# Kernel tuning notes

Hardware: AMD Instinct MI355X
Metric: run time of the kernel (lower is better)

The kernel has to match this reference:

```python
import jax, jax.numpy as jnp
import numpy as np

N_NODES = 100000
N_EDGES = 1600000
IN_F, OUT_F = 25, 50


def setup_inputs() -> dict:
    key = jax.random.key(0)
    k1, k2, k3, k4 = jax.random.split(key, 4)
    x = jax.random.normal(k1, (N_NODES, IN_F), dtype=jnp.float32)
    W = jax.random.normal(k2, (IN_F, OUT_F), dtype=jnp.float32) * (1.0 / np.sqrt(IN_F))
    b = jax.random.normal(k3, (OUT_F,), dtype=jnp.float32) * 0.01
    edge_index = jax.random.randint(k4, (2, N_EDGES), 0, N_NODES, dtype=jnp.int64)
    return {"x": x, "W": W, "b": b, "edge_index": edge_index}


def reference(x, W, b, edge_index):
    # GCNConv(normalize=False): linear transform, then add-aggregate over edges, + bias.
    src, dst = edge_index[0], edge_index[1]
    h = x @ W                                   # [N, OUT_F] small dense GEMM
    msgs = h[src]                               # [E, OUT_F] irregular gather
    agg = jax.ops.segment_sum(msgs, dst, num_segments=N_NODES)  # scatter-add to targets
    out = agg + b
    return jax.nn.relu(out)
```

## Files before the change

### kernel.cpp

```cpp
#include <hip/hip_runtime.h>

#define N_NODES 100000
#define N_EDGES 1600000
#define IN_F 25
#define OUT_F 50

#define BNODES 98
#define NBUCK 1024
#define DL_SHIFT 7
#define SLAB 1920
#define BIN_NB 98
#define BIN_CHUNK 16384
#define XPREP_ITEMS (N_NODES * 16)
#define PREP_GRID 512

__global__ __launch_bounds__(1024) void gcn_prep_kernel(
        const float* __restrict__ x,
        const int* __restrict__ ei,
        int* __restrict__ gfill,
        unsigned* __restrict__ recs,
        unsigned* __restrict__ xb) {
    __shared__ int lcnt[NBUCK];
    __shared__ int lbase[NBUCK];
    int tid = threadIdx.x, bid = blockIdx.x;
    if (bid < BIN_NB) {
        for (int i = tid; i < NBUCK; i += 1024) lcnt[i] = 0;
        __syncthreads();
        const int4* s4 = (const int4*)ei;
        const int4* d4 = (const int4*)(ei + N_EDGES);
        int base4 = bid * (BIN_CHUNK / 4);
        int4 sv[4], dv[4];
        bool ok[4];
#pragma unroll
        for (int k = 0; k < 4; ++k) {
            int i4 = base4 + k * 1024 + tid;
            ok[k] = (i4 < N_EDGES / 4);
            if (ok[k]) { dv[k] = d4[i4]; sv[k] = s4[i4]; }
        }
#pragma unroll
        for (int k = 0; k < 4; ++k) {
            if (ok[k]) {
                const int* dd = &dv[k].x;
#pragma unroll
                for (int c = 0; c < 4; ++c)
                    atomicAdd(&lcnt[((unsigned)dd[c]) / BNODES], 1);
            }
        }
        __syncthreads();
        for (int i = tid; i < NBUCK; i += 1024) {
            int c = lcnt[i];
            lbase[i] = c ? atomicAdd(&gfill[i], c) : 0;
            lcnt[i] = 0;
        }
        __syncthreads();
#pragma unroll
        for (int k = 0; k < 4; ++k) {
            if (ok[k]) {
                const int* dd = &dv[k].x;
                const int* ss = &sv[k].x;
#pragma unroll
                for (int c = 0; c < 4; ++c) {
                    unsigned d = (unsigned)dd[c], s = (unsigned)ss[c];
                    unsigned bk = d / BNODES;
                    unsigned dl = d - bk * BNODES;
                    int p = lbase[bk] + atomicAdd(&lcnt[bk], 1);
                    if ((unsigned)p < SLAB)
                        recs[bk * SLAB + p] = (s << DL_SHIFT) | dl;
                }
            }
        }
    } else {
        for (int idx = (bid - BIN_NB) * 1024 + tid; idx < XPREP_ITEMS;
             idx += (PREP_GRID - BIN_NB) * 1024) {
            int n  = idx >> 4;
            int fp = (idx & 15) * 2;
            float v0 = (fp < IN_F) ? x[n * IN_F + fp] : 0.f;
            float v1 = (fp + 1 < IN_F) ? x[n * IN_F + fp + 1] : 0.f;
            union { float fl; unsigned u; } a, c;
            a.fl = v0; c.fl = v1;
            unsigned r0 = (a.u + 0x7FFFu + ((a.u >> 16) & 1u)) >> 16;
            unsigned r1 = (c.u + 0x7FFFu + ((c.u >> 16) & 1u)) >> 16;
            xb[idx] = (r1 << 16) | (r0 & 0xFFFFu);
        }
    }
}

__global__ __launch_bounds__(512, 8) void gcn_k3_kernel(
        const uint4* __restrict__ xb4,
        const unsigned* __restrict__ recs,
        const int* __restrict__ gfill,
        const float* __restrict__ W,
        const float* __restrict__ b,
        float* __restrict__ out) {
    __shared__ unsigned raw[SLAB];
    __shared__ int      srt[SLAB];
    __shared__ int      cnt[128], fil[128];
    __shared__ int      offs[BNODES + 1];
    __shared__ float    acc[BNODES * IN_F];
    __shared__ float    Ws[IN_F * OUT_F];
    __shared__ float    bs[OUT_F];

    int bk = blockIdx.x, tid = threadIdx.x;
    if (tid < 128) { cnt[tid] = 0; fil[tid] = 0; }
    for (int i = tid; i < IN_F * OUT_F; i += 512) Ws[i] = W[i];
    if (tid < OUT_F) bs[tid] = b[tid];
    __syncthreads();

    int cntE = min(gfill[bk], SLAB);
    const unsigned* rb = recs + bk * SLAB;

    for (int j = tid; j < cntE; j += 512) {
        unsigned rec = rb[j];
        raw[j] = rec;
        atomicAdd(&cnt[rec & ((1 << DL_SHIFT) - 1)], 1);
    }
    __syncthreads();

    if (tid < 64) {
        int v = cnt[tid];
        for (int off = 1; off < 64; off <<= 1) {
            int t = __shfl_up(v, off, 64);
            if (tid >= off) v += t;
        }
        offs[tid + 1] = v;
        int t64 = __shfl(v, 63, 64);
        int v2 = (tid < BNODES - 64) ? cnt[64 + tid] : 0;
        for (int off = 1; off < 64; off <<= 1) {
            int t = __shfl_up(v2, off, 64);
            if (tid >= off) v2 += t;
        }
        if (tid < BNODES - 64) offs[65 + tid] = t64 + v2;
        if (tid == 0) offs[0] = 0;
    }
    __syncthreads();

    for (int j = tid; j < cntE; j += 512) {
        unsigned rec = raw[j];
        int dl = rec & ((1 << DL_SHIFT) - 1);
        int p = offs[dl] + atomicAdd(&fil[dl], 1);
        srt[p] = (int)(rec >> DL_SHIFT);
    }
    __syncthreads();

    {
        int g = tid >> 2, f = tid & 3;
        if (g < BNODES) {
            int e0 = offs[g], e1 = offs[g + 1];
            float a0 = 0.f, a1 = 0.f, a2 = 0.f, a3 = 0.f;
            float a4 = 0.f, a5 = 0.f, a6 = 0.f, a7 = 0.f;
            int j = e0;
            for (; j + 4 <= e1; j += 4) {
                uint4 u[4];
#pragma unroll
                for (int q = 0; q < 4; ++q) u[q] = xb4[srt[j + q] * 4 + f];
#pragma unroll
                for (int q = 0; q < 4; ++q) {
                    union { unsigned uu; float fl; } t0, t1, t2, t3, t4, t5, t6, t7;
                    t0.uu = u[q].x << 16; t1.uu = u[q].x & 0xFFFF0000u;
                    t2.uu = u[q].y << 16; t3.uu = u[q].y & 0xFFFF0000u;
                    t4.uu = u[q].z << 16; t5.uu = u[q].z & 0xFFFF0000u;
                    t6.uu = u[q].w << 16; t7.uu = u[q].w & 0xFFFF0000u;
                    a0 += t0.fl; a1 += t1.fl; a2 += t2.fl; a3 += t3.fl;
                    a4 += t4.fl; a5 += t5.fl; a6 += t6.fl; a7 += t7.fl;
                }
            }
            for (; j < e1; ++j) {
                uint4 u = xb4[srt[j] * 4 + f];
                union { unsigned uu; float fl; } t0, t1, t2, t3, t4, t5, t6, t7;
                t0.uu = u.x << 16; t1.uu = u.x & 0xFFFF0000u;
                t2.uu = u.y << 16; t3.uu = u.y & 0xFFFF0000u;
                t4.uu = u.z << 16; t5.uu = u.z & 0xFFFF0000u;
                t6.uu = u.w << 16; t7.uu = u.w & 0xFFFF0000u;
                a0 += t0.fl; a1 += t1.fl; a2 += t2.fl; a3 += t3.fl;
                a4 += t4.fl; a5 += t5.fl; a6 += t6.fl; a7 += t7.fl;
            }
            int ff = 8 * f;
            float av[8] = {a0, a1, a2, a3, a4, a5, a6, a7};
#pragma unroll
            for (int k = 0; k < 8; ++k)
                if (ff + k < IN_F) acc[g * IN_F + ff + k] = av[k];
        }
    }
    __syncthreads();

    int node0 = bk * BNODES;
    for (int i = tid; i < BNODES * OUT_F; i += 512) {
        int nl = i / OUT_F;
        int o  = i - nl * OUT_F;
        int node = node0 + nl;
        if (node < N_NODES) {
            float a = bs[o];
#pragma unroll
            for (int k = 0; k < IN_F; ++k)
                a += acc[nl * IN_F + k] * Ws[k * OUT_F + o];
            out[node * OUT_F + o] = fmaxf(a, 0.f);
        }
    }
}

extern "C" void kernel_launch(void* const* d_in, const int* in_sizes, int n_in,
                              void* d_out, int out_size, void* d_ws, size_t ws_size,
                              hipStream_t stream) {
    const float* x  = (const float*)d_in[0];
    const float* W  = (const float*)d_in[1];
    const float* b  = (const float*)d_in[2];
    const int*   ei = (const int*)d_in[3];
    float* out = (float*)d_out;

    char* ws = (char*)d_ws;
    unsigned* xb    = (unsigned*)(ws);
    unsigned* recs  = (unsigned*)(ws + 6400000);
    int*      gfill = (int*)(ws + 14264576);

    hipMemsetAsync(gfill, 0, NBUCK * sizeof(int), stream);
    gcn_prep_kernel<<<PREP_GRID, 1024, 0, stream>>>(x, ei, gfill, recs, xb);
    gcn_k3_kernel<<<NBUCK, 512, 0, stream>>>((const uint4*)xb, recs, gfill, W, b, out);
}
```

Before: 128.5 us.

## Register-tile final GEMM with padded float4 weights and rebalance edge binning blocks

The final dense transform now has each thread compute a 2-node by 4-output tile, reading weights as float4 from a shared copy padded to 52 columns and storing results as float2. This cuts shared-memory loads and the per-element divide compared with the old one-output-per-thread loop. Edge binning is also spread across 128 blocks of 3125 int4 slots instead of 98 blocks of 4096, which balances load and frees the tail. The risk is more register pressure in the epilogue and fewer blocks left for the x-to-bf16 conversion.

Measured after the change: 358.6 us. 179% more time.

```diff
diff --git a/kernel.cpp b/kernel.cpp
--- a/kernel.cpp
+++ b/kernel.cpp
@@ -9,10 +9,12 @@
 #define NBUCK 1024
 #define DL_SHIFT 7
 #define SLAB 1920
-#define BIN_NB 98
-#define BIN_CHUNK 16384
+#define BIN_NB 128
+#define I4_TOTAL (N_EDGES / 4)
+#define I4_PER_BLK 3125
 #define XPREP_ITEMS (N_NODES * 16)
 #define PREP_GRID 512
+#define WPAD 52
 
 __global__ __launch_bounds__(1024) void gcn_prep_kernel(
         const float* __restrict__ x,
@@ -28,14 +30,14 @@
         __syncthreads();
         const int4* s4 = (const int4*)ei;
         const int4* d4 = (const int4*)(ei + N_EDGES);
-        int base4 = bid * (BIN_CHUNK / 4);
+        int base4 = bid * I4_PER_BLK;
         int4 sv[4], dv[4];
         bool ok[4];
 #pragma unroll
         for (int k = 0; k < 4; ++k) {
-            int i4 = base4 + k * 1024 + tid;
-            ok[k] = (i4 < N_EDGES / 4);
-            if (ok[k]) { dv[k] = d4[i4]; sv[k] = s4[i4]; }
+            int slot = k * 1024 + tid;
+            ok[k] = (slot < I4_PER_BLK);
+            if (ok[k]) { dv[k] = d4[base4 + slot]; sv[k] = s4[base4 + slot]; }
         }
 #pragma unroll
         for (int k = 0; k < 4; ++k) {
@@ -97,13 +99,16 @@
     __shared__ int      cnt[128], fil[128];
     __shared__ int      offs[BNODES + 1];
     __shared__ float    acc[BNODES * IN_F];
-    __shared__ float    Ws[IN_F * OUT_F];
-    __shared__ float    bs[OUT_F];
+    __shared__ __align__(16) float Ws[IN_F * WPAD];
+    __shared__ float    bs[WPAD];
 
     int bk = blockIdx.x, tid = threadIdx.x;
     if (tid < 128) { cnt[tid] = 0; fil[tid] = 0; }
-    for (int i = tid; i < IN_F * OUT_F; i += 512) Ws[i] = W[i];
-    if (tid < OUT_F) bs[tid] = b[tid];
+    for (int i = tid; i < IN_F * WPAD; i += 512) {
+        int r = i / WPAD, c = i - r * WPAD;
+        Ws[i] = (c < OUT_F) ? W[r * OUT_F + c] : 0.f;
+    }
+    if (tid < WPAD) bs[tid] = (tid < OUT_F) ? b[tid] : 0.f;
     __syncthreads();
 
     int cntE = min(gfill[bk], SLAB);
@@ -184,16 +189,40 @@
     __syncthreads();
 
     int node0 = bk * BNODES;
-    for (int i = tid; i < BNODES * OUT_F; i += 512) {
-        int nl = i / OUT_F;
-        int o  = i - nl * OUT_F;
-        int node = node0 + nl;
-        if (node < N_NODES) {
-            float a = bs[o];
-#pragma unroll
-            for (int k = 0; k < IN_F; ++k)
-                a += acc[nl * IN_F + k] * Ws[k * OUT_F + o];
-            out[node * OUT_F + o] = fmaxf(a, 0.f);
+    for (int i = tid; i < 49 * 13; i += 512) {
+        int p  = i / 13;
+        int oc = i - p * 13;
+        int o  = oc * 4;
+        int nl0 = 2 * p, nl1 = 2 * p + 1;
+        float a00 = bs[o], a01 = bs[o + 1], a02 = bs[o + 2], a03 = bs[o + 3];
+        float a10 = a00, a11 = a01, a12 = a02, a13 = a03;
+#pragma unroll
+        for (int k = 0; k < IN_F; ++k) {
+            float av0 = acc[nl0 * IN_F + k];
+            float av1 = acc[nl1 * IN_F + k];
+            float4 w = *reinterpret_cast<const float4*>(&Ws[k * WPAD + o]);
+            a00 = fmaf(av0, w.x, a00); a01 = fmaf(av0, w.y, a01);
+            a02 = fmaf(av0, w.z, a02); a03 = fmaf(av0, w.w, a03);
+            a10 = fmaf(av1, w.x, a10); a11 = fmaf(av1, w.y, a11);
+            a12 = fmaf(av1, w.z, a12); a13 = fmaf(av1, w.w, a13);
+        }
+        int n0 = node0 + nl0, n1 = node0 + nl1;
+        bool full = (oc < 12);
+        if (n0 < N_NODES) {
+            float2 r0; r0.x = fmaxf(a00, 0.f); r0.y = fmaxf(a01, 0.f);
+            *reinterpret_cast<float2*>(&out[n0 * OUT_F + o]) = r0;
+            if (full) {
+                float2 r1; r1.x = fmaxf(a02, 0.f); r1.y = fmaxf(a03, 0.f);
+                *reinterpret_cast<float2*>(&out[n0 * OUT_F + o + 2]) = r1;
+            }
+        }
+        if (n1 < N_NODES) {
+            float2 r0; r0.x = fmaxf(a10, 0.f); r0.y = fmaxf(a11, 0.f);
+            *reinterpret_cast<float2*>(&out[n1 * OUT_F + o]) = r0;
+            if (full) {
+                float2 r1; r1.x = fmaxf(a12, 0.f); r1.y = fmaxf(a13, 0.f);
+                *reinterpret_cast<float2*>(&out[n1 * OUT_F + o + 2]) = r1;
+            }
         }
     }
 }
```
